# Performance work log

Measured on AMD Instinct MI355X. Metric: run time of the kernel, lower is better.

## Reference

```python
import jax, jax.numpy as jnp
import numpy as np

B, N, C, R, E = 8, 4096, 128, 16, 65536


def setup_inputs() -> dict:
    key = jax.random.key(0)
    ks = jax.random.split(key, 8)
    node_features = jax.random.normal(ks[0], (B, N, C), dtype=jnp.float32)
    edge_index = jax.random.randint(ks[1], (B, 2, E), 0, N, dtype=jnp.int64)
    edge_type = jax.random.randint(ks[2], (B, E), 0, R, dtype=jnp.int64)
    s = 1.0 / np.sqrt(C)
    rel_weight = jax.random.uniform(ks[3], (R, C, C), jnp.float32, -s, s)
    root_weight = jax.random.uniform(ks[4], (C, C), jnp.float32, -s, s)
    rgcn_bias = jnp.zeros((C,), jnp.float32)
    lin_weight = jax.random.uniform(ks[5], (C, 1), jnp.float32, -s, s)
    lin_bias = jnp.zeros((1,), jnp.float32)
    return {
        'node_features': node_features,
        'edge_index': edge_index,
        'edge_type': edge_type,
        'rel_weight': rel_weight,
        'root_weight': root_weight,
        'rgcn_bias': rgcn_bias,
        'lin_weight': lin_weight,
        'lin_bias': lin_bias,
    }


def _rgcn_score(node_features, edge_index, edge_type, rel_weight, root_weight,
                rgcn_bias, lin_weight, lin_bias):
    # Flatten batch of graphs into one big disjoint graph (as batch_rgcn does).
    x = node_features.reshape(B * N, C)
    offs = (jnp.arange(B, dtype=edge_index.dtype) * N)[:, None, None]  # (B,1,1)
    ei = (edge_index + offs).transpose(1, 0, 2).reshape(2, B * E)  # (2, B*E)
    et = edge_type.reshape(B * E)
    src, dst = ei[0], ei[1]

    x_src = x[src]  # (B*E, C) gathered source features
    # root transform + bias (RGCNConv root_weight + bias)
    out = x @ root_weight + rgcn_bias  # (B*N, C)
    # per-relation mean aggregation; mean(W_r x_j) == W_r mean(x_j)
    for r in range(R):
        mask = (et == r).astype(x.dtype)  # (B*E,)
        s = jax.ops.segment_sum(x_src * mask[:, None], dst, num_segments=B * N)
        cnt = jax.ops.segment_sum(mask, dst, num_segments=B * N)
        mean = jnp.where(cnt[:, None] > 0, s / jnp.maximum(cnt, 1.0)[:, None], 0.0)
        out = out + mean @ rel_weight[r]

    out = jax.nn.relu(out)  # dropout is identity at eval
    scores = (out @ lin_weight + lin_bias).reshape(B, N)
    return scores


def reference(node_features, edge_index, edge_type, rel_weight, root_weight,
              rgcn_bias, lin_weight, lin_bias):
    return _rgcn_score(node_features, edge_index, edge_type, rel_weight,
                       root_weight, rgcn_bias, lin_weight, lin_bias)
```

## Files before the change

### kernel.cpp

```cpp
#include <hip/hip_runtime.h>

#define BB 8
#define NN 4096
#define CC 128
#define RR 16
#define EE 65536
#define NNODES 32768
#define NEDGES 524288
#define BCAP  48
#define SCAP  16
#define NT    32
#define ALP   136

typedef unsigned short ushort_t;
typedef short bf16x8 __attribute__((ext_vector_type(8)));
typedef float f32x4 __attribute__((ext_vector_type(4)));

__device__ __forceinline__ unsigned short f2b(float f) {
    unsigned u = __builtin_bit_cast(unsigned, f);
    unsigned r = (u + 0x7fffu + ((u >> 16) & 1u)) >> 16;
    return (unsigned short)r;
}
__device__ __forceinline__ float b2f(unsigned short s) {
    return __builtin_bit_cast(float, (unsigned)s << 16);
}
__device__ __forceinline__ float ldf(const void* p, int j, int isbf) {
    return isbf ? b2f(((const ushort_t*)p)[j]) : ((const float*)p)[j];
}
__device__ __forceinline__ int ldi(const int* p, int j, int is64) {
    return p[j << is64];
}
__device__ __forceinline__ unsigned cvtpk(float lo, float hi) {
    unsigned r;
    asm("v_cvt_pk_bf16_f32 %0, %1, %2" : "=v"(r) : "v"(lo), "v"(hi));
    return r;
}

__device__ __forceinline__ int probe_isbf(const ushort_t* xf) {
    int t = threadIdx.x & 63;
    int bad = 0;
    for (int j = t; j < 512; j += 64) {
        unsigned e = (xf[j] >> 7) & 0xffu;
        if (e >= 160u) bad = 1;
    }
    return __ballot(bad) == 0ull;
}

#define GATHER_SUM(u, sb) do { \
    s[sb+0] += __builtin_bit_cast(float, (u).x << 16); \
    s[sb+1] += __builtin_bit_cast(float, (u).x & 0xffff0000u); \
    s[sb+2] += __builtin_bit_cast(float, (u).y << 16); \
    s[sb+3] += __builtin_bit_cast(float, (u).y & 0xffff0000u); \
    s[sb+4] += __builtin_bit_cast(float, (u).z << 16); \
    s[sb+5] += __builtin_bit_cast(float, (u).z & 0xffff0000u); \
    s[sb+6] += __builtin_bit_cast(float, (u).w << 16); \
    s[sb+7] += __builtin_bit_cast(float, (u).w & 0xffff0000u); \
} while (0)

__global__ __launch_bounds__(256) void prep_k(const void* __restrict__ x,
                                              const void* __restrict__ relw,
                                              const void* __restrict__ rootw,
                                              const int* __restrict__ ei,
                                              const int* __restrict__ et,
                                              ushort_t* __restrict__ Xb,
                                              ushort_t* __restrict__ WT3,
                                              int* __restrict__ dcnt,
                                              int* __restrict__ bucket,
                                              int* __restrict__ flags) {
    int bx = blockIdx.x, t = threadIdx.x;
    if (bx < 512) {
        int lane = t & 63;
        int pa = (lane < 16) ? ei[2 * lane + 1] : 0;
        int pb = (lane < 16) ? et[2 * lane + 1] : 0;
        int w64i = (__ballot(pa != 0) == 0ull);
        int w64t = (__ballot(pb != 0) == 0ull);
        int b = bx & 7;
        #pragma unroll
        for (int i = 0; i < 4; ++i) {
            int e = (bx >> 3) * 1024 + i * 256 + t;
            int src = ldi(ei, (b * 2) * EE + e, w64i);
            int dst = ldi(ei, (b * 2 + 1) * EE + e, w64i);
            int r = ldi(et, (b << 16) + e, w64t);
            int gd = (b << 12) + dst;
            int pos = atomicAdd(&dcnt[gd], 1);
            if (pos < BCAP)
                bucket[gd * BCAP + pos] = (((b << 12) + src) << 4) | r;
        }
    } else if (bx < 1024) {
        int isbf = probe_isbf((const ushort_t*)x);
        int bx2 = bx - 512;
        int base = (bx2 & 7) * 65536 + (bx2 >> 3) * 256 + t;
        #pragma unroll
        for (int i = 0; i < 4; ++i) {
            int tid = base + i * 16384;
            if (isbf) {
                ((uint4*)Xb)[tid] = ((const uint4*)x)[tid];
            } else {
                const float4* xf = (const float4*)x;
                float4 a = xf[2 * tid], b = xf[2 * tid + 1];
                ushort4 o0, o1;
                o0.x = f2b(a.x); o0.y = f2b(a.y); o0.z = f2b(a.z); o0.w = f2b(a.w);
                o1.x = f2b(b.x); o1.y = f2b(b.y); o1.z = f2b(b.z); o1.w = f2b(b.w);
                ((ushort4*)Xb)[2 * tid] = o0; ((ushort4*)Xb)[2 * tid + 1] = o1;
            }
        }
    } else {
        __shared__ ushort_t Ls[128 * 40];
        int isbf = probe_isbf((const ushort_t*)x);
        int mb = bx - 1024;
        int mat = mb >> 2, chunk = mb & 3;
        const void* src = (mat == 16) ? rootw : relw;
        int soff = (mat == 16) ? 0 : mat * 16384;
        int k0 = chunk * 32;
        #pragma unroll
        for (int i = 0; i < 16; ++i) {
            int idx = t + i * 256;
            int k = idx >> 7, c = idx & 127;
            Ls[c * 40 + k] = f2b(ldf(src, soff + (k0 + k) * 128 + c, isbf));
        }
        __syncthreads();
        #pragma unroll
        for (int i = 0; i < 2; ++i) {
            int idx = t + i * 256;
            int cg = idx >> 6, lane = idx & 63;
            int lrow = lane & 15, lq = lane >> 4;
            uint4 v = *(const uint4*)(&Ls[(cg * 16 + lrow) * 40 + lq * 8]);
            *(uint4*)(WT3 + ((size_t)((mat * 4 + chunk) * 8 + cg)) * 512 + lane * 8) = v;
        }
        if (mb == 0 && t == 0) flags[0] = isbf;
    }
}

__global__ __launch_bounds__(256, 4) void agg_k(const ushort_t* __restrict__ Xb,
                                                const ushort_t* __restrict__ WT3,
                                                const int* __restrict__ dcnt,
                                                const int* __restrict__ bucket,
                                                const void* __restrict__ bias,
                                                const void* __restrict__ linw,
                                                const void* __restrict__ linb,
                                                void* __restrict__ out,
                                                const int* __restrict__ flags) {
    __shared__ int scnt[NT * 16];
    __shared__ ushort_t srt[NT * 16 * SCAP];
    __shared__ ushort_t A[2][NT * ALP];
    __shared__ float red[NT][5];
    int bx = blockIdx.x, t = threadIdx.x;
    int isbf = flags[0];
    int n0 = (bx & 7) * NN + (bx >> 3) * NT;

    scnt[t] = 0; scnt[256 + t] = 0;
    __syncthreads();

    int nsub = t >> 3, tsub = t & 7;
    int gn = n0 + nsub;
    int offA = tsub * 8, offB = 64 + tsub * 8;
    int nc = dcnt[gn]; if (nc > BCAP) nc = BCAP;
    const int* bk = bucket + gn * BCAP;
    for (int j = tsub; j < nc; j += 8) {
        int v = bk[j];
        int pos = atomicAdd(&scnt[(nsub << 4) + (v & 15)], 1);
        if (pos < SCAP)
            srt[(((nsub << 4) + (v & 15)) << 4) + pos] = (ushort_t)((unsigned)v >> 4);
    }
    __syncthreads();

    int wave = t >> 6, lane = t & 63, lrow = lane & 15, lq = lane >> 4;
    f32x4 acc[2][2] = {};

    {
        int cf = scnt[nsub << 4];
        int ce = cf > SCAP ? SCAP : cf;
        const ushort_t* lst = &srt[nsub << 8];
        float s[16];
        #pragma unroll
        for (int j = 0; j < 16; ++j) s[j] = 0.f;
        for (int e = 0; e < ce; ++e) {
            const ushort_t* xr = Xb + (size_t)lst[e] * 128;
            uint4 ua = *(const uint4*)(xr + offA), ub = *(const uint4*)(xr + offB);
            GATHER_SUM(ua, 0); GATHER_SUM(ub, 8);
        }
        float w = (cf > 0) ? 1.0f / (float)cf : 0.f;
        uint4 va, vb;
        va.x = cvtpk(s[0] * w, s[1] * w);   va.y = cvtpk(s[2] * w, s[3] * w);
        va.z = cvtpk(s[4] * w, s[5] * w);   va.w = cvtpk(s[6] * w, s[7] * w);
        vb.x = cvtpk(s[8] * w, s[9] * w);   vb.y = cvtpk(s[10] * w, s[11] * w);
        vb.z = cvtpk(s[12] * w, s[13] * w); vb.w = cvtpk(s[14] * w, s[15] * w);
        *(uint4*)(&A[0][nsub * ALP + offA]) = va;
        *(uint4*)(&A[0][nsub * ALP + offB]) = vb;
    }
    __syncthreads();

    for (int p = 0; p < 17; ++p) {
        int np = p + 1;
        uint4 r0a, r0b, r1a, r1b, r2a, r2b, r3a, r3b;
        int cf = 0, ce = 0;
        if (np < 16) {
            cf = scnt[(nsub << 4) + np];
            ce = cf > SCAP ? SCAP : cf;
            uint4 q0 = *(const uint4*)(&srt[((nsub << 4) + np) << 4]);
            int e0 = q0.x & 0xffffu, e1 = q0.x >> 16;
            int e2i = q0.y & 0xffffu, e3 = q0.y >> 16;
            if (ce > 0) { const ushort_t* xr = Xb + (size_t)e0 * 128;  r0a = *(const uint4*)(xr + offA); r0b = *(const uint4*)(xr + offB); }
            if (ce > 1) { const ushort_t* xr = Xb + (size_t)e1 * 128;  r1a = *(const uint4*)(xr + offA); r1b = *(const uint4*)(xr + offB); }
            if (ce > 2) { const ushort_t* xr = Xb + (size_t)e2i * 128; r2a = *(const uint4*)(xr + offA); r2b = *(const uint4*)(xr + offB); }
            if (ce > 3) { const ushort_t* xr = Xb + (size_t)e3 * 128;  r3a = *(const uint4*)(xr + offA); r3b = *(const uint4*)(xr + offB); }
        } else if (np == 16) {
            const ushort_t* xr = Xb + (size_t)gn * 128;
            r0a = *(const uint4*)(xr + offA); r0b = *(const uint4*)(xr + offB);
        }
        const ushort_t* Ap = A[p & 1];
        const ushort_t* bw = WT3 + (size_t)p * 16384 + (wave * 2) * 512 + lane * 8;
        __builtin_amdgcn_s_setprio(1);
        #pragma unroll
        for (int ks = 0; ks < 4; ++ks) {
            int k0 = ks * 32 + lq * 8;
            bf16x8 a0 = *(const bf16x8*)(&Ap[lrow * ALP + k0]);
            bf16x8 a1 = *(const bf16x8*)(&Ap[(16 + lrow) * ALP + k0]);
            bf16x8 b0 = *(const bf16x8*)(bw + ks * 4096);
            bf16x8 b1 = *(const bf16x8*)(bw + ks * 4096 + 512);
            acc[0][0] = __builtin_amdgcn_mfma_f32_16x16x32_bf16(a0, b0, acc[0][0], 0, 0, 0);
            acc[0][1] = __builtin_amdgcn_mfma_f32_16x16x32_bf16(a0, b1, acc[0][1], 0, 0, 0);
            acc[1][0] = __builtin_amdgcn_mfma_f32_16x16x32_bf16(a1, b0, acc[1][0], 0, 0, 0);
            acc[1][1] = __builtin_amdgcn_mfma_f32_16x16x32_bf16(a1, b1, acc[1][1], 0, 0, 0);
        }
        __builtin_amdgcn_s_setprio(0);
        if (np < 16) {
            float s[16];
            #pragma unroll
            for (int j = 0; j < 16; ++j) s[j] = 0.f;
            if (ce > 0) { GATHER_SUM(r0a, 0); GATHER_SUM(r0b, 8); }
            if (ce > 1) { GATHER_SUM(r1a, 0); GATHER_SUM(r1b, 8); }
            if (ce > 2) { GATHER_SUM(r2a, 0); GATHER_SUM(r2b, 8); }
            if (ce > 3) { GATHER_SUM(r3a, 0); GATHER_SUM(r3b, 8); }
            if (ce > 4) {
                const ushort_t* lst = &srt[((nsub << 4) + np) << 4];
                for (int e4 = 4; e4 < ce; ++e4) {
                    const ushort_t* xr = Xb + (size_t)lst[e4] * 128;
                    uint4 ta = *(const uint4*)(xr + offA), tb = *(const uint4*)(xr + offB);
                    GATHER_SUM(ta, 0); GATHER_SUM(tb, 8);
                }
            }
            float w = (cf > 0) ? 1.0f / (float)cf : 0.f;
            uint4 va, vb;
            va.x = cvtpk(s[0] * w, s[1] * w);   va.y = cvtpk(s[2] * w, s[3] * w);
            va.z = cvtpk(s[4] * w, s[5] * w);   va.w = cvtpk(s[6] * w, s[7] * w);
            vb.x = cvtpk(s[8] * w, s[9] * w);   vb.y = cvtpk(s[10] * w, s[11] * w);
            vb.z = cvtpk(s[12] * w, s[13] * w); vb.w = cvtpk(s[14] * w, s[15] * w);
            *(uint4*)(&A[np & 1][nsub * ALP + offA]) = va;
            *(uint4*)(&A[np & 1][nsub * ALP + offB]) = vb;
        } else if (np == 16) {
            *(uint4*)(&A[np & 1][nsub * ALP + offA]) = r0a;
            *(uint4*)(&A[np & 1][nsub * ALP + offB]) = r0b;
        }
        if (p < 16) __syncthreads();
    }

    int wn = wave << 5;
    int c0 = wn + lrow, c1 = wn + 16 + lrow;
    float bi0 = ldf(bias, c0, isbf), bi1 = ldf(bias, c1, isbf);
    float lw0 = ldf(linw, c0, isbf), lw1 = ldf(linw, c1, isbf);
    #pragma unroll
    for (int mi = 0; mi < 2; ++mi)
        #pragma unroll
        for (int rg = 0; rg < 4; ++rg) {
            float p = fmaxf(acc[mi][0][rg] + bi0, 0.f) * lw0
                    + fmaxf(acc[mi][1][rg] + bi1, 0.f) * lw1;
            p += __shfl_xor(p, 1, 64);
            p += __shfl_xor(p, 2, 64);
            p += __shfl_xor(p, 4, 64);
            p += __shfl_xor(p, 8, 64);
            if (lrow == 0) red[mi * 16 + lq * 4 + rg][wave] = p;
        }
    __syncthreads();
    if (t < NT) {
        float res = red[t][0] + red[t][1] + red[t][2] + red[t][3] + ldf(linb, 0, isbf);
        if (isbf) ((ushort_t*)out)[n0 + t] = f2b(res);
        else      ((float*)out)[n0 + t] = res;
    }
}

extern "C" void kernel_launch(void* const* d_in, const int* in_sizes, int n_in,
                              void* d_out, int out_size, void* d_ws, size_t ws_size,
                              hipStream_t stream) {
    const void* x     = d_in[0];
    const int*  ei    = (const int*)d_in[1];
    const int*  et    = (const int*)d_in[2];
    const void* relw  = d_in[3];
    const void* rootw = d_in[4];
    const void* bias  = d_in[5];
    const void* linw  = d_in[6];
    const void* linb  = d_in[7];

    const size_t WS_NEED = 15368448;
    if (ws_size < WS_NEED) return;

    char* ws = (char*)d_ws;
    ushort_t* Xb     = (ushort_t*)(ws);
    ushort_t* WT3    = (ushort_t*)(ws + 8388608);
    int*      dcnt   = (int*)(ws + 8945664);
    int*      bucket = (int*)(ws + 9076736);
    int*      flags  = (int*)(ws + 15368192);

    hipMemsetAsync(dcnt, 0, 131072, stream);
    prep_k<<<1092, 256, 0, stream>>>(x, relw, rootw, ei, et, Xb, WT3, dcnt, bucket, flags);
    agg_k<<<1024, 256, 0, stream>>>(Xb, WT3, dcnt, bucket, bias, linw, linb, d_out, flags);
}
```

Before: 144.4 us.

## Fuse prep and aggregation into one persistent kernel with grid barriers

```diff
diff --git a/kernel.cpp b/kernel.cpp
--- a/kernel.cpp
+++ b/kernel.cpp
@@ -8,9 +8,10 @@
 #define NNODES 32768
 #define NEDGES 524288
 #define BCAP  48
-#define SCAP  16
+#define SCE   15
 #define NT    32
 #define ALP   136
+#define NBLK  1024
 
 typedef unsigned short ushort_t;
 typedef short bf16x8 __attribute__((ext_vector_type(8)));
@@ -36,17 +37,7 @@
     return r;
 }
 
-__device__ __forceinline__ int probe_isbf(const ushort_t* xf) {
-    int t = threadIdx.x & 63;
-    int bad = 0;
-    for (int j = t; j < 512; j += 64) {
-        unsigned e = (xf[j] >> 7) & 0xffu;
-        if (e >= 160u) bad = 1;
-    }
-    return __ballot(bad) == 0ull;
-}
-
-#define GATHER_SUM(u, sb) do { \
+#define GSUM8(u, sb) do { \
     s[sb+0] += __builtin_bit_cast(float, (u).x << 16); \
     s[sb+1] += __builtin_bit_cast(float, (u).x & 0xffff0000u); \
     s[sb+2] += __builtin_bit_cast(float, (u).y << 16); \
@@ -57,127 +48,131 @@
     s[sb+7] += __builtin_bit_cast(float, (u).w & 0xffff0000u); \
 } while (0)
 
-__global__ __launch_bounds__(256) void prep_k(const void* __restrict__ x,
-                                              const void* __restrict__ relw,
-                                              const void* __restrict__ rootw,
-                                              const int* __restrict__ ei,
-                                              const int* __restrict__ et,
-                                              ushort_t* __restrict__ Xb,
-                                              ushort_t* __restrict__ WT3,
-                                              int* __restrict__ dcnt,
-                                              int* __restrict__ bucket,
-                                              int* __restrict__ flags) {
-    int bx = blockIdx.x, t = threadIdx.x;
-    if (bx < 512) {
-        int lane = t & 63;
-        int pa = (lane < 16) ? ei[2 * lane + 1] : 0;
-        int pb = (lane < 16) ? et[2 * lane + 1] : 0;
-        int w64i = (__ballot(pa != 0) == 0ull);
-        int w64t = (__ballot(pb != 0) == 0ull);
-        int b = bx & 7;
-        #pragma unroll
-        for (int i = 0; i < 4; ++i) {
-            int e = (bx >> 3) * 1024 + i * 256 + t;
-            int src = ldi(ei, (b * 2) * EE + e, w64i);
-            int dst = ldi(ei, (b * 2 + 1) * EE + e, w64i);
-            int r = ldi(et, (b << 16) + e, w64t);
-            int gd = (b << 12) + dst;
-            int pos = atomicAdd(&dcnt[gd], 1);
-            if (pos < BCAP)
-                bucket[gd * BCAP + pos] = (((b << 12) + src) << 4) | r;
-        }
-    } else if (bx < 1024) {
-        int isbf = probe_isbf((const ushort_t*)x);
-        int bx2 = bx - 512;
-        int base = (bx2 & 7) * 65536 + (bx2 >> 3) * 256 + t;
-        #pragma unroll
-        for (int i = 0; i < 4; ++i) {
-            int tid = base + i * 16384;
-            if (isbf) {
-                ((uint4*)Xb)[tid] = ((const uint4*)x)[tid];
-            } else {
-                const float4* xf = (const float4*)x;
-                float4 a = xf[2 * tid], b = xf[2 * tid + 1];
-                ushort4 o0, o1;
-                o0.x = f2b(a.x); o0.y = f2b(a.y); o0.z = f2b(a.z); o0.w = f2b(a.w);
-                o1.x = f2b(b.x); o1.y = f2b(b.y); o1.z = f2b(b.z); o1.w = f2b(b.w);
-                ((ushort4*)Xb)[2 * tid] = o0; ((ushort4*)Xb)[2 * tid + 1] = o1;
-            }
-        }
-    } else {
-        __shared__ ushort_t Ls[128 * 40];
-        int isbf = probe_isbf((const ushort_t*)x);
-        int mb = bx - 1024;
-        int mat = mb >> 2, chunk = mb & 3;
-        const void* src = (mat == 16) ? rootw : relw;
-        int soff = (mat == 16) ? 0 : mat * 16384;
-        int k0 = chunk * 32;
-        #pragma unroll
-        for (int i = 0; i < 16; ++i) {
-            int idx = t + i * 256;
-            int k = idx >> 7, c = idx & 127;
-            Ls[c * 40 + k] = f2b(ldf(src, soff + (k0 + k) * 128 + c, isbf));
-        }
-        __syncthreads();
-        #pragma unroll
-        for (int i = 0; i < 2; ++i) {
-            int idx = t + i * 256;
-            int cg = idx >> 6, lane = idx & 63;
-            int lrow = lane & 15, lq = lane >> 4;
-            uint4 v = *(const uint4*)(&Ls[(cg * 16 + lrow) * 40 + lq * 8]);
-            *(uint4*)(WT3 + ((size_t)((mat * 4 + chunk) * 8 + cg)) * 512 + lane * 8) = v;
-        }
-        if (mb == 0 && t == 0) flags[0] = isbf;
-    }
-}
-
-__global__ __launch_bounds__(256, 4) void agg_k(const ushort_t* __restrict__ Xb,
-                                                const ushort_t* __restrict__ WT3,
-                                                const int* __restrict__ dcnt,
-                                                const int* __restrict__ bucket,
-                                                const void* __restrict__ bias,
-                                                const void* __restrict__ linw,
-                                                const void* __restrict__ linb,
-                                                void* __restrict__ out,
-                                                const int* __restrict__ flags) {
-    __shared__ int scnt[NT * 16];
-    __shared__ ushort_t srt[NT * 16 * SCAP];
-    __shared__ ushort_t A[2][NT * ALP];
-    __shared__ float red[NT][5];
-    int bx = blockIdx.x, t = threadIdx.x;
-    int isbf = flags[0];
+struct AggSM {
+    int scnt[NT * 16];
+    ushort_t srt[NT * 16 * 16];
+    ushort_t A[2][NT * ALP];
+    float red[NT][5];
+};
+union SM {
+    AggSM agg;
+    ushort_t Ls[128 * 40];
+};
+
+__device__ __forceinline__ void gbar(int* bar, int idx) {
+    __syncthreads();
+    if (threadIdx.x == 0) {
+        __threadfence();
+        atomicAdd(&bar[idx * 16], 1);
+        while (atomicAdd(&bar[idx * 16], 0) < NBLK)
+            __builtin_amdgcn_s_sleep(8);
+        __threadfence();
+    }
+    __syncthreads();
+}
+
+__device__ __forceinline__ void do_cast(int bx, int t, const void* x,
+                                        ushort_t* Xb, int isbf) {
+    int base = (bx & 7) * 65536 + (bx >> 3) * 512 + t;
+    #pragma unroll
+    for (int i = 0; i < 2; ++i) {
+        int tid = base + i * 256;
+        if (isbf) {
+            ((uint4*)Xb)[tid] = ((const uint4*)x)[tid];
+        } else {
+            const float4* xf = (const float4*)x;
+            float4 a = xf[2 * tid], b = xf[2 * tid + 1];
+            ushort4 o0, o1;
+            o0.x = f2b(a.x); o0.y = f2b(a.y); o0.z = f2b(a.z); o0.w = f2b(a.w);
+            o1.x = f2b(b.x); o1.y = f2b(b.y); o1.z = f2b(b.z); o1.w = f2b(b.w);
+            ((ushort4*)Xb)[2 * tid] = o0; ((ushort4*)Xb)[2 * tid + 1] = o1;
+        }
+    }
+}
+
+__device__ __forceinline__ void do_wt3(int mb, int t, ushort_t* Ls,
+                                       const void* relw, const void* rootw,
+                                       ushort_t* WT3, int isbf) {
+    int mat = mb >> 2, chunk = mb & 3;
+    const void* src = (mat == 16) ? rootw : relw;
+    int soff = (mat == 16) ? 0 : mat * 16384;
+    int k0 = chunk * 32;
+    #pragma unroll
+    for (int i = 0; i < 16; ++i) {
+        int idx = t + i * 256;
+        int k = idx >> 7, c = idx & 127;
+        Ls[c * 40 + k] = f2b(ldf(src, soff + (k0 + k) * 128 + c, isbf));
+    }
+    __syncthreads();
+    #pragma unroll
+    for (int i = 0; i < 2; ++i) {
+        int idx = t + i * 256;
+        int cg = idx >> 6, lane = idx & 63;
+        int lrow = lane & 15, lq = lane >> 4;
+        uint4 v = *(const uint4*)(&Ls[(cg * 16 + lrow) * 40 + lq * 8]);
+        *(uint4*)(WT3 + ((size_t)((mat * 4 + chunk) * 8 + cg)) * 512 + lane * 8) = v;
+    }
+}
+
+__device__ __forceinline__ void do_edges(int bx, int t, const int* ei, const int* et,
+                                         int* dcnt, int* bucket, int w64i, int w64t) {
+    int b = bx & 7;
+    int e0 = (bx >> 3) * 512 + t, e1 = e0 + 256;
+    int src0 = ldi(ei, (b * 2) * EE + e0, w64i);
+    int dst0 = ldi(ei, (b * 2 + 1) * EE + e0, w64i);
+    int r0 = ldi(et, (b << 16) + e0, w64t);
+    int src1 = ldi(ei, (b * 2) * EE + e1, w64i);
+    int dst1 = ldi(ei, (b * 2 + 1) * EE + e1, w64i);
+    int r1 = ldi(et, (b << 16) + e1, w64t);
+    int gd0 = (b << 12) + dst0, gd1 = (b << 12) + dst1;
+    int p0 = atomicAdd(&dcnt[gd0 << 4], 1);
+    int p1 = atomicAdd(&dcnt[gd1 << 4], 1);
+    if (p0 < BCAP) bucket[gd0 * BCAP + p0] = (((b << 12) + src0) << 4) | r0;
+    if (p1 < BCAP) bucket[gd1 * BCAP + p1] = (((b << 12) + src1) << 4) | r1;
+}
+
+__device__ __forceinline__ void do_agg(int bx, int t, AggSM& sm,
+                                       const ushort_t* Xb, const ushort_t* WT3,
+                                       const int* dcnt, const int* bucket,
+                                       const void* bias, const void* linw,
+                                       const void* linb, void* out, int isbf) {
     int n0 = (bx & 7) * NN + (bx >> 3) * NT;
 
-    scnt[t] = 0; scnt[256 + t] = 0;
+    sm.scnt[t] = 0; sm.scnt[256 + t] = 0;
     __syncthreads();
 
     int nsub = t >> 3, tsub = t & 7;
     int gn = n0 + nsub;
     int offA = tsub * 8, offB = 64 + tsub * 8;
-    int nc = dcnt[gn]; if (nc > BCAP) nc = BCAP;
+    int nc = dcnt[gn << 4]; if (nc > BCAP) nc = BCAP;
     const int* bk = bucket + gn * BCAP;
     for (int j = tsub; j < nc; j += 8) {
         int v = bk[j];
-        int pos = atomicAdd(&scnt[(nsub << 4) + (v & 15)], 1);
-        if (pos < SCAP)
-            srt[(((nsub << 4) + (v & 15)) << 4) + pos] = (ushort_t)((unsigned)v >> 4);
-    }
+        int row = (nsub << 4) + (v & 15);
+        int pos = atomicAdd(&sm.scnt[row], 1);
+        if (pos < SCE)
+            sm.srt[(row << 4) + 1 + pos] = (ushort_t)((unsigned)v >> 4);
+    }
+    __syncthreads();
+    sm.srt[t << 4] = (ushort_t)sm.scnt[t];
+    sm.srt[(t + 256) << 4] = (ushort_t)sm.scnt[t + 256];
     __syncthreads();
 
     int wave = t >> 6, lane = t & 63, lrow = lane & 15, lq = lane >> 4;
     f32x4 acc[2][2] = {};
 
     {
-        int cf = scnt[nsub << 4];
-        int ce = cf > SCAP ? SCAP : cf;
-        const ushort_t* lst = &srt[nsub << 8];
+        int row = nsub << 4;
+        uint4 q0 = *(const uint4*)(&sm.srt[row << 4]);
+        int cf = q0.x & 0xffffu; int ce = cf > SCE ? SCE : cf;
         float s[16];
         #pragma unroll
         for (int j = 0; j < 16; ++j) s[j] = 0.f;
         for (int e = 0; e < ce; ++e) {
-            const ushort_t* xr = Xb + (size_t)lst[e] * 128;
+            int gs = sm.srt[(row << 4) + 1 + e];
+            const ushort_t* xr = Xb + (size_t)gs * 128;
             uint4 ua = *(const uint4*)(xr + offA), ub = *(const uint4*)(xr + offB);
-            GATHER_SUM(ua, 0); GATHER_SUM(ub, 8);
+            GSUM8(ua, 0); GSUM8(ub, 8);
         }
         float w = (cf > 0) ? 1.0f / (float)cf : 0.f;
         uint4 va, vb;
@@ -185,30 +180,29 @@
         va.z = cvtpk(s[4] * w, s[5] * w);   va.w = cvtpk(s[6] * w, s[7] * w);
         vb.x = cvtpk(s[8] * w, s[9] * w);   vb.y = cvtpk(s[10] * w, s[11] * w);
         vb.z = cvtpk(s[12] * w, s[13] * w); vb.w = cvtpk(s[14] * w, s[15] * w);
-        *(uint4*)(&A[0][nsub * ALP + offA]) = va;
-        *(uint4*)(&A[0][nsub * ALP + offB]) = vb;
+        *(uint4*)(&sm.A[0][nsub * ALP + offA]) = va;
+        *(uint4*)(&sm.A[0][nsub * ALP + offB]) = vb;
     }
     __syncthreads();
 
     for (int p = 0; p < 17; ++p) {
         int np = p + 1;
         uint4 r0a, r0b, r1a, r1b, r2a, r2b, r3a, r3b;
-        int cf = 0, ce = 0;
+        int cf = 0, ce = 0, row = 0;
         if (np < 16) {
-            cf = scnt[(nsub << 4) + np];
-            ce = cf > SCAP ? SCAP : cf;
-            uint4 q0 = *(const uint4*)(&srt[((nsub << 4) + np) << 4]);
-            int e0 = q0.x & 0xffffu, e1 = q0.x >> 16;
-            int e2i = q0.y & 0xffffu, e3 = q0.y >> 16;
-            if (ce > 0) { const ushort_t* xr = Xb + (size_t)e0 * 128;  r0a = *(const uint4*)(xr + offA); r0b = *(const uint4*)(xr + offB); }
-            if (ce > 1) { const ushort_t* xr = Xb + (size_t)e1 * 128;  r1a = *(const uint4*)(xr + offA); r1b = *(const uint4*)(xr + offB); }
-            if (ce > 2) { const ushort_t* xr = Xb + (size_t)e2i * 128; r2a = *(const uint4*)(xr + offA); r2b = *(const uint4*)(xr + offB); }
-            if (ce > 3) { const ushort_t* xr = Xb + (size_t)e3 * 128;  r3a = *(const uint4*)(xr + offA); r3b = *(const uint4*)(xr + offB); }
+            row = (nsub << 4) + np;
+            uint4 q0 = *(const uint4*)(&sm.srt[row << 4]);
+            cf = q0.x & 0xffffu; ce = cf > SCE ? SCE : cf;
+            int e0 = q0.x >> 16, e1 = q0.y & 0xffffu, e2 = q0.y >> 16, e3 = q0.z & 0xffffu;
+            if (ce > 0) { const ushort_t* xr = Xb + (size_t)e0 * 128; r0a = *(const uint4*)(xr + offA); r0b = *(const uint4*)(xr + offB); }
+            if (ce > 1) { const ushort_t* xr = Xb + (size_t)e1 * 128; r1a = *(const uint4*)(xr + offA); r1b = *(const uint4*)(xr + offB); }
+            if (ce > 2) { const ushort_t* xr = Xb + (size_t)e2 * 128; r2a = *(const uint4*)(xr + offA); r2b = *(const uint4*)(xr + offB); }
+            if (ce > 3) { const ushort_t* xr = Xb + (size_t)e3 * 128; r3a = *(const uint4*)(xr + offA); r3b = *(const uint4*)(xr + offB); }
         } else if (np == 16) {
             const ushort_t* xr = Xb + (size_t)gn * 128;
             r0a = *(const uint4*)(xr + offA); r0b = *(const uint4*)(xr + offB);
         }
-        const ushort_t* Ap = A[p & 1];
+        const ushort_t* Ap = sm.A[p & 1];
         const ushort_t* bw = WT3 + (size_t)p * 16384 + (wave * 2) * 512 + lane * 8;
         __builtin_amdgcn_s_setprio(1);
         #pragma unroll
@@ -228,16 +222,16 @@
             float s[16];
             #pragma unroll
             for (int j = 0; j < 16; ++j) s[j] = 0.f;
-            if (ce > 0) { GATHER_SUM(r0a, 0); GATHER_SUM(r0b, 8); }
-            if (ce > 1) { GATHER_SUM(r1a, 0); GATHER_SUM(r1b, 8); }
-            if (ce > 2) { GATHER_SUM(r2a, 0); GATHER_SUM(r2b, 8); }
-            if (ce > 3) { GATHER_SUM(r3a, 0); GATHER_SUM(r3b, 8); }
+            if (ce > 0) { GSUM8(r0a, 0); GSUM8(r0b, 8); }
+            if (ce > 1) { GSUM8(r1a, 0); GSUM8(r1b, 8); }
+            if (ce > 2) { GSUM8(r2a, 0); GSUM8(r2b, 8); }
+            if (ce > 3) { GSUM8(r3a, 0); GSUM8(r3b, 8); }
             if (ce > 4) {
-                const ushort_t* lst = &srt[((nsub << 4) + np) << 4];
                 for (int e4 = 4; e4 < ce; ++e4) {
-                    const ushort_t* xr = Xb + (size_t)lst[e4] * 128;
+                    int gs = sm.srt[(row << 4) + 1 + e4];
+                    const ushort_t* xr = Xb + (size_t)gs * 128;
                     uint4 ta = *(const uint4*)(xr + offA), tb = *(const uint4*)(xr + offB);
-                    GATHER_SUM(ta, 0); GATHER_SUM(tb, 8);
+                    GSUM8(ta, 0); GSUM8(tb, 8);
                 }
             }
             float w = (cf > 0) ? 1.0f / (float)cf : 0.f;
@@ -246,11 +240,11 @@
             va.z = cvtpk(s[4] * w, s[5] * w);   va.w = cvtpk(s[6] * w, s[7] * w);
             vb.x = cvtpk(s[8] * w, s[9] * w);   vb.y = cvtpk(s[10] * w, s[11] * w);
             vb.z = cvtpk(s[12] * w, s[13] * w); vb.w = cvtpk(s[14] * w, s[15] * w);
-            *(uint4*)(&A[np & 1][nsub * ALP + offA]) = va;
-            *(uint4*)(&A[np & 1][nsub * ALP + offB]) = vb;
+            *(uint4*)(&sm.A[np & 1][nsub * ALP + offA]) = va;
+            *(uint4*)(&sm.A[np & 1][nsub * ALP + offB]) = vb;
         } else if (np == 16) {
-            *(uint4*)(&A[np & 1][nsub * ALP + offA]) = r0a;
-            *(uint4*)(&A[np & 1][nsub * ALP + offB]) = r0b;
+            *(uint4*)(&sm.A[np & 1][nsub * ALP + offA]) = r0a;
+            *(uint4*)(&sm.A[np & 1][nsub * ALP + offB]) = r0b;
         }
         if (p < 16) __syncthreads();
     }
@@ -269,14 +263,44 @@
             p += __shfl_xor(p, 2, 64);
             p += __shfl_xor(p, 4, 64);
             p += __shfl_xor(p, 8, 64);
-            if (lrow == 0) red[mi * 16 + lq * 4 + rg][wave] = p;
+            if (lrow == 0) sm.red[mi * 16 + lq * 4 + rg][wave] = p;
         }
     __syncthreads();
     if (t < NT) {
-        float res = red[t][0] + red[t][1] + red[t][2] + red[t][3] + ldf(linb, 0, isbf);
+        float res = sm.red[t][0] + sm.red[t][1] + sm.red[t][2] + sm.red[t][3]
+                  + ldf(linb, 0, isbf);
         if (isbf) ((ushort_t*)out)[n0 + t] = f2b(res);
         else      ((float*)out)[n0 + t] = res;
     }
+}
+
+__global__ __launch_bounds__(256, 4) void fused_k(const void* __restrict__ x,
+                                                  const void* __restrict__ relw,
+                                                  const void* __restrict__ rootw,
+                                                  const int* __restrict__ ei,
+                                                  const int* __restrict__ et,
+                                                  ushort_t* __restrict__ Xb,
+                                                  ushort_t* __restrict__ WT3,
+                                                  int* __restrict__ dcnt,
+                                                  int* __restrict__ bucket,
+                                                  int* __restrict__ bar,
+                                                  const void* __restrict__ bias,
+                                                  const void* __restrict__ linw,
+                                                  const void* __restrict__ linb,
+                                                  void* __restrict__ out,
+                                                  int isbf, int w64i, int w64t) {
+    __shared__ SM sm;
+    int bx = blockIdx.x, t = threadIdx.x;
+
+    if (t < 128) ((uint4*)dcnt)[(bx << 7) + t] = make_uint4(0, 0, 0, 0);
+    do_cast(bx, t, x, Xb, isbf);
+    if (bx < 68) do_wt3(bx, t, sm.Ls, relw, rootw, WT3, isbf);
+    gbar(bar, 0);
+
+    do_edges(bx, t, ei, et, dcnt, bucket, w64i, w64t);
+    gbar(bar, 1);
+
+    do_agg(bx, t, sm.agg, Xb, WT3, dcnt, bucket, bias, linw, linb, out, isbf);
 }
 
 extern "C" void kernel_launch(void* const* d_in, const int* in_sizes, int n_in,
@@ -291,17 +315,21 @@
     const void* linw  = d_in[6];
     const void* linb  = d_in[7];
 
-    const size_t WS_NEED = 15368448;
+    int isbf = (in_sizes[0] == BB * NN * CC * 2);
+    int w64i = (in_sizes[1] == BB * 2 * EE * 8);
+    int w64t = (in_sizes[2] == BB * EE * 8);
+
+    const size_t WS_NEED = 17334528;
     if (ws_size < WS_NEED) return;
 
     char* ws = (char*)d_ws;
     ushort_t* Xb     = (ushort_t*)(ws);
     ushort_t* WT3    = (ushort_t*)(ws + 8388608);
     int*      dcnt   = (int*)(ws + 8945664);
-    int*      bucket = (int*)(ws + 9076736);
-    int*      flags  = (int*)(ws + 15368192);
-
-    hipMemsetAsync(dcnt, 0, 131072, stream);
-    prep_k<<<1092, 256, 0, stream>>>(x, relw, rootw, ei, et, Xb, WT3, dcnt, bucket, flags);
-    agg_k<<<1024, 256, 0, stream>>>(Xb, WT3, dcnt, bucket, bias, linw, linb, d_out, flags);
-}
+    int*      bucket = (int*)(ws + 11042816);
+    int*      bar    = (int*)(ws + 17334272);
+
+    hipMemsetAsync(bar, 0, 256, stream);
+    fused_k<<<NBLK, 256, 0, stream>>>(x, relw, rootw, ei, et, Xb, WT3, dcnt, bucket,
+                                      bar, bias, linw, linb, d_out, isbf, w64i, w64t);
+}
```

New measurement: 381.3 us. 2.64x slower.

## Warp-specialize aggregation into gather and MFMA waves, pad counters, host-side dtype detection

Applied to the files above, without the earlier changes.

```diff
diff --git a/kernel.cpp b/kernel.cpp
--- a/kernel.cpp
+++ b/kernel.cpp
@@ -8,7 +8,7 @@
 #define NNODES 32768
 #define NEDGES 524288
 #define BCAP  48
-#define SCAP  16
+#define SCE   15
 #define NT    32
 #define ALP   136
 
@@ -36,17 +36,7 @@
     return r;
 }
 
-__device__ __forceinline__ int probe_isbf(const ushort_t* xf) {
-    int t = threadIdx.x & 63;
-    int bad = 0;
-    for (int j = t; j < 512; j += 64) {
-        unsigned e = (xf[j] >> 7) & 0xffu;
-        if (e >= 160u) bad = 1;
-    }
-    return __ballot(bad) == 0ull;
-}
-
-#define GATHER_SUM(u, sb) do { \
+#define GSUM8(u, sb) do { \
     s[sb+0] += __builtin_bit_cast(float, (u).x << 16); \
     s[sb+1] += __builtin_bit_cast(float, (u).x & 0xffff0000u); \
     s[sb+2] += __builtin_bit_cast(float, (u).y << 16); \
@@ -66,14 +56,9 @@
                                               ushort_t* __restrict__ WT3,
                                               int* __restrict__ dcnt,
                                               int* __restrict__ bucket,
-                                              int* __restrict__ flags) {
+                                              int isbf, int w64i, int w64t) {
     int bx = blockIdx.x, t = threadIdx.x;
     if (bx < 512) {
-        int lane = t & 63;
-        int pa = (lane < 16) ? ei[2 * lane + 1] : 0;
-        int pb = (lane < 16) ? et[2 * lane + 1] : 0;
-        int w64i = (__ballot(pa != 0) == 0ull);
-        int w64t = (__ballot(pb != 0) == 0ull);
         int b = bx & 7;
         #pragma unroll
         for (int i = 0; i < 4; ++i) {
@@ -82,12 +67,11 @@
             int dst = ldi(ei, (b * 2 + 1) * EE + e, w64i);
             int r = ldi(et, (b << 16) + e, w64t);
             int gd = (b << 12) + dst;
-            int pos = atomicAdd(&dcnt[gd], 1);
+            int pos = atomicAdd(&dcnt[gd << 4], 1);
             if (pos < BCAP)
                 bucket[gd * BCAP + pos] = (((b << 12) + src) << 4) | r;
         }
     } else if (bx < 1024) {
-        int isbf = probe_isbf((const ushort_t*)x);
         int bx2 = bx - 512;
         int base = (bx2 & 7) * 65536 + (bx2 >> 3) * 256 + t;
         #pragma unroll
@@ -106,7 +90,6 @@
         }
     } else {
         __shared__ ushort_t Ls[128 * 40];
-        int isbf = probe_isbf((const ushort_t*)x);
         int mb = bx - 1024;
         int mat = mb >> 2, chunk = mb & 3;
         const void* src = (mat == 16) ? rootw : relw;
@@ -127,11 +110,10 @@
             uint4 v = *(const uint4*)(&Ls[(cg * 16 + lrow) * 40 + lq * 8]);
             *(uint4*)(WT3 + ((size_t)((mat * 4 + chunk) * 8 + cg)) * 512 + lane * 8) = v;
         }
-        if (mb == 0 && t == 0) flags[0] = isbf;
-    }
-}
-
-__global__ __launch_bounds__(256, 4) void agg_k(const ushort_t* __restrict__ Xb,
+    }
+}
+
+__global__ __launch_bounds__(512, 4) void agg_k(const ushort_t* __restrict__ Xb,
                                                 const ushort_t* __restrict__ WT3,
                                                 const int* __restrict__ dcnt,
                                                 const int* __restrict__ bucket,
@@ -139,45 +121,53 @@
                                                 const void* __restrict__ linw,
                                                 const void* __restrict__ linb,
                                                 void* __restrict__ out,
-                                                const int* __restrict__ flags) {
+                                                int isbf) {
     __shared__ int scnt[NT * 16];
-    __shared__ ushort_t srt[NT * 16 * SCAP];
+    __shared__ ushort_t srt[NT * 16 * 16];
     __shared__ ushort_t A[2][NT * ALP];
     __shared__ float red[NT][5];
     int bx = blockIdx.x, t = threadIdx.x;
-    int isbf = flags[0];
     int n0 = (bx & 7) * NN + (bx >> 3) * NT;
 
-    scnt[t] = 0; scnt[256 + t] = 0;
-    __syncthreads();
-
-    int nsub = t >> 3, tsub = t & 7;
+    scnt[t & 511] = 0;
+    __syncthreads();
+
+    {
+        int ns16 = t >> 4, ts16 = t & 15;
+        int gn16 = n0 + ns16;
+        int nc = dcnt[gn16 << 4]; if (nc > BCAP) nc = BCAP;
+        const int* bk = bucket + gn16 * BCAP;
+        for (int j = ts16; j < nc; j += 16) {
+            int v = bk[j];
+            int row = (ns16 << 4) + (v & 15);
+            int pos = atomicAdd(&scnt[row], 1);
+            if (pos < SCE)
+                srt[(row << 4) + 1 + pos] = (ushort_t)((unsigned)v >> 4);
+        }
+    }
+    __syncthreads();
+    srt[t << 4] = (ushort_t)scnt[t];
+    __syncthreads();
+
+    int wave = t >> 6, lane = t & 63, lrow = lane & 15, lq = lane >> 4;
+    int tg = t & 255;
+    int nsub = tg >> 3, tsub = tg & 7;
     int gn = n0 + nsub;
     int offA = tsub * 8, offB = 64 + tsub * 8;
-    int nc = dcnt[gn]; if (nc > BCAP) nc = BCAP;
-    const int* bk = bucket + gn * BCAP;
-    for (int j = tsub; j < nc; j += 8) {
-        int v = bk[j];
-        int pos = atomicAdd(&scnt[(nsub << 4) + (v & 15)], 1);
-        if (pos < SCAP)
-            srt[(((nsub << 4) + (v & 15)) << 4) + pos] = (ushort_t)((unsigned)v >> 4);
-    }
-    __syncthreads();
-
-    int wave = t >> 6, lane = t & 63, lrow = lane & 15, lq = lane >> 4;
     f32x4 acc[2][2] = {};
 
-    {
-        int cf = scnt[nsub << 4];
-        int ce = cf > SCAP ? SCAP : cf;
-        const ushort_t* lst = &srt[nsub << 8];
+    if (wave >= 4) {
+        int row = nsub << 4;
+        uint4 q0 = *(const uint4*)(&srt[row << 4]);
+        int cf = q0.x & 0xffffu; int ce = cf > SCE ? SCE : cf;
         float s[16];
         #pragma unroll
         for (int j = 0; j < 16; ++j) s[j] = 0.f;
         for (int e = 0; e < ce; ++e) {
-            const ushort_t* xr = Xb + (size_t)lst[e] * 128;
+            int gs = srt[(row << 4) + 1 + e];
+            const ushort_t* xr = Xb + (size_t)gs * 128;
             uint4 ua = *(const uint4*)(xr + offA), ub = *(const uint4*)(xr + offB);
-            GATHER_SUM(ua, 0); GATHER_SUM(ub, 8);
+            GSUM8(ua, 0); GSUM8(ub, 8);
         }
         float w = (cf > 0) ? 1.0f / (float)cf : 0.f;
         uint4 va, vb;
@@ -192,52 +182,46 @@
 
     for (int p = 0; p < 17; ++p) {
         int np = p + 1;
-        uint4 r0a, r0b, r1a, r1b, r2a, r2b, r3a, r3b;
-        int cf = 0, ce = 0;
-        if (np < 16) {
-            cf = scnt[(nsub << 4) + np];
-            ce = cf > SCAP ? SCAP : cf;
-            uint4 q0 = *(const uint4*)(&srt[((nsub << 4) + np) << 4]);
-            int e0 = q0.x & 0xffffu, e1 = q0.x >> 16;
-            int e2i = q0.y & 0xffffu, e3 = q0.y >> 16;
-            if (ce > 0) { const ushort_t* xr = Xb + (size_t)e0 * 128;  r0a = *(const uint4*)(xr + offA); r0b = *(const uint4*)(xr + offB); }
-            if (ce > 1) { const ushort_t* xr = Xb + (size_t)e1 * 128;  r1a = *(const uint4*)(xr + offA); r1b = *(const uint4*)(xr + offB); }
-            if (ce > 2) { const ushort_t* xr = Xb + (size_t)e2i * 128; r2a = *(const uint4*)(xr + offA); r2b = *(const uint4*)(xr + offB); }
-            if (ce > 3) { const ushort_t* xr = Xb + (size_t)e3 * 128;  r3a = *(const uint4*)(xr + offA); r3b = *(const uint4*)(xr + offB); }
-        } else if (np == 16) {
-            const ushort_t* xr = Xb + (size_t)gn * 128;
-            r0a = *(const uint4*)(xr + offA); r0b = *(const uint4*)(xr + offB);
-        }
-        const ushort_t* Ap = A[p & 1];
-        const ushort_t* bw = WT3 + (size_t)p * 16384 + (wave * 2) * 512 + lane * 8;
-        __builtin_amdgcn_s_setprio(1);
-        #pragma unroll
-        for (int ks = 0; ks < 4; ++ks) {
-            int k0 = ks * 32 + lq * 8;
-            bf16x8 a0 = *(const bf16x8*)(&Ap[lrow * ALP + k0]);
-            bf16x8 a1 = *(const bf16x8*)(&Ap[(16 + lrow) * ALP + k0]);
-            bf16x8 b0 = *(const bf16x8*)(bw + ks * 4096);
-            bf16x8 b1 = *(const bf16x8*)(bw + ks * 4096 + 512);
-            acc[0][0] = __builtin_amdgcn_mfma_f32_16x16x32_bf16(a0, b0, acc[0][0], 0, 0, 0);
-            acc[0][1] = __builtin_amdgcn_mfma_f32_16x16x32_bf16(a0, b1, acc[0][1], 0, 0, 0);
-            acc[1][0] = __builtin_amdgcn_mfma_f32_16x16x32_bf16(a1, b0, acc[1][0], 0, 0, 0);
-            acc[1][1] = __builtin_amdgcn_mfma_f32_16x16x32_bf16(a1, b1, acc[1][1], 0, 0, 0);
-        }
-        __builtin_amdgcn_s_setprio(0);
-        if (np < 16) {
+        if (wave < 4) {
+            const ushort_t* Ap = A[p & 1];
+            const ushort_t* bw = WT3 + (size_t)p * 16384 + (wave * 2) * 512 + lane * 8;
+            __builtin_amdgcn_s_setprio(1);
+            #pragma unroll
+            for (int ks = 0; ks < 4; ++ks) {
+                int k0 = ks * 32 + lq * 8;
+                bf16x8 a0 = *(const bf16x8*)(&Ap[lrow * ALP + k0]);
+                bf16x8 a1 = *(const bf16x8*)(&Ap[(16 + lrow) * ALP + k0]);
+                bf16x8 b0 = *(const bf16x8*)(bw + ks * 4096);
+                bf16x8 b1 = *(const bf16x8*)(bw + ks * 4096 + 512);
+                acc[0][0] = __builtin_amdgcn_mfma_f32_16x16x32_bf16(a0, b0, acc[0][0], 0, 0, 0);
+                acc[0][1] = __builtin_amdgcn_mfma_f32_16x16x32_bf16(a0, b1, acc[0][1], 0, 0, 0);
+                acc[1][0] = __builtin_amdgcn_mfma_f32_16x16x32_bf16(a1, b0, acc[1][0], 0, 0, 0);
+                acc[1][1] = __builtin_amdgcn_mfma_f32_16x16x32_bf16(a1, b1, acc[1][1], 0, 0, 0);
+            }
+            __builtin_amdgcn_s_setprio(0);
+        } else if (np < 16) {
+            int row = (nsub << 4) + np;
+            uint4 q0 = *(const uint4*)(&srt[row << 4]);
+            int cf = q0.x & 0xffffu; int ce = cf > SCE ? SCE : cf;
+            int e0 = q0.x >> 16, e1 = q0.y & 0xffffu, e2 = q0.y >> 16, e3 = q0.z & 0xffffu;
+            uint4 r0a, r0b, r1a, r1b, r2a, r2b, r3a, r3b;
+            if (ce > 0) { const ushort_t* xr = Xb + (size_t)e0 * 128; r0a = *(const uint4*)(xr + offA); r0b = *(const uint4*)(xr + offB); }
+            if (ce > 1) { const ushort_t* xr = Xb + (size_t)e1 * 128; r1a = *(const uint4*)(xr + offA); r1b = *(const uint4*)(xr + offB); }
+            if (ce > 2) { const ushort_t* xr = Xb + (size_t)e2 * 128; r2a = *(const uint4*)(xr + offA); r2b = *(const uint4*)(xr + offB); }
+            if (ce > 3) { const ushort_t* xr = Xb + (size_t)e3 * 128; r3a = *(const uint4*)(xr + offA); r3b = *(const uint4*)(xr + offB); }
             float s[16];
             #pragma unroll
             for (int j = 0; j < 16; ++j) s[j] = 0.f;
-            if (ce > 0) { GATHER_SUM(r0a, 0); GATHER_SUM(r0b, 8); }
-            if (ce > 1) { GATHER_SUM(r1a, 0); GATHER_SUM(r1b, 8); }
-            if (ce > 2) { GATHER_SUM(r2a, 0); GATHER_SUM(r2b, 8); }
-            if (ce > 3) { GATHER_SUM(r3a, 0); GATHER_SUM(r3b, 8); }
+            if (ce > 0) { GSUM8(r0a, 0); GSUM8(r0b, 8); }
+            if (ce > 1) { GSUM8(r1a, 0); GSUM8(r1b, 8); }
+            if (ce > 2) { GSUM8(r2a, 0); GSUM8(r2b, 8); }
+            if (ce > 3) { GSUM8(r3a, 0); GSUM8(r3b, 8); }
             if (ce > 4) {
-                const ushort_t* lst = &srt[((nsub << 4) + np) << 4];
                 for (int e4 = 4; e4 < ce; ++e4) {
-                    const ushort_t* xr = Xb + (size_t)lst[e4] * 128;
+                    int gs = srt[(row << 4) + 1 + e4];
+                    const ushort_t* xr = Xb + (size_t)gs * 128;
                     uint4 ta = *(const uint4*)(xr + offA), tb = *(const uint4*)(xr + offB);
-                    GATHER_SUM(ta, 0); GATHER_SUM(tb, 8);
+                    GSUM8(ta, 0); GSUM8(tb, 8);
                 }
             }
             float w = (cf > 0) ? 1.0f / (float)cf : 0.f;
@@ -249,28 +233,32 @@
             *(uint4*)(&A[np & 1][nsub * ALP + offA]) = va;
             *(uint4*)(&A[np & 1][nsub * ALP + offB]) = vb;
         } else if (np == 16) {
+            const ushort_t* xr = Xb + (size_t)gn * 128;
+            uint4 r0a = *(const uint4*)(xr + offA), r0b = *(const uint4*)(xr + offB);
             *(uint4*)(&A[np & 1][nsub * ALP + offA]) = r0a;
             *(uint4*)(&A[np & 1][nsub * ALP + offB]) = r0b;
         }
         if (p < 16) __syncthreads();
     }
 
-    int wn = wave << 5;
-    int c0 = wn + lrow, c1 = wn + 16 + lrow;
-    float bi0 = ldf(bias, c0, isbf), bi1 = ldf(bias, c1, isbf);
-    float lw0 = ldf(linw, c0, isbf), lw1 = ldf(linw, c1, isbf);
-    #pragma unroll
-    for (int mi = 0; mi < 2; ++mi)
-        #pragma unroll
-        for (int rg = 0; rg < 4; ++rg) {
-            float p = fmaxf(acc[mi][0][rg] + bi0, 0.f) * lw0
-                    + fmaxf(acc[mi][1][rg] + bi1, 0.f) * lw1;
-            p += __shfl_xor(p, 1, 64);
-            p += __shfl_xor(p, 2, 64);
-            p += __shfl_xor(p, 4, 64);
-            p += __shfl_xor(p, 8, 64);
-            if (lrow == 0) red[mi * 16 + lq * 4 + rg][wave] = p;
-        }
+    if (wave < 4) {
+        int wn = wave << 5;
+        int c0 = wn + lrow, c1 = wn + 16 + lrow;
+        float bi0 = ldf(bias, c0, isbf), bi1 = ldf(bias, c1, isbf);
+        float lw0 = ldf(linw, c0, isbf), lw1 = ldf(linw, c1, isbf);
+        #pragma unroll
+        for (int mi = 0; mi < 2; ++mi)
+            #pragma unroll
+            for (int rg = 0; rg < 4; ++rg) {
+                float p = fmaxf(acc[mi][0][rg] + bi0, 0.f) * lw0
+                        + fmaxf(acc[mi][1][rg] + bi1, 0.f) * lw1;
+                p += __shfl_xor(p, 1, 64);
+                p += __shfl_xor(p, 2, 64);
+                p += __shfl_xor(p, 4, 64);
+                p += __shfl_xor(p, 8, 64);
+                if (lrow == 0) red[mi * 16 + lq * 4 + rg][wave] = p;
+            }
+    }
     __syncthreads();
     if (t < NT) {
         float res = red[t][0] + red[t][1] + red[t][2] + red[t][3] + ldf(linb, 0, isbf);
@@ -291,17 +279,21 @@
     const void* linw  = d_in[6];
     const void* linb  = d_in[7];
 
-    const size_t WS_NEED = 15368448;
+    int isbf = (in_sizes[0] == BB * NN * CC * 2);
+    int w64i = (in_sizes[1] == BB * 2 * EE * 8);
+    int w64t = (in_sizes[2] == BB * EE * 8);
+
+    const size_t WS_NEED = 17334272;
     if (ws_size < WS_NEED) return;
 
     char* ws = (char*)d_ws;
     ushort_t* Xb     = (ushort_t*)(ws);
     ushort_t* WT3    = (ushort_t*)(ws + 8388608);
     int*      dcnt   = (int*)(ws + 8945664);
-    int*      bucket = (int*)(ws + 9076736);
-    int*      flags  = (int*)(ws + 15368192);
-
-    hipMemsetAsync(dcnt, 0, 131072, stream);
-    prep_k<<<1092, 256, 0, stream>>>(x, relw, rootw, ei, et, Xb, WT3, dcnt, bucket, flags);
-    agg_k<<<1024, 256, 0, stream>>>(Xb, WT3, dcnt, bucket, bias, linw, linb, d_out, flags);
-}
+    int*      bucket = (int*)(ws + 11042816);
+
+    hipMemsetAsync(dcnt, 0, 2097152, stream);
+    prep_k<<<1092, 256, 0, stream>>>(x, relw, rootw, ei, et, Xb, WT3, dcnt, bucket,
+                                     isbf, w64i, w64t);
+    agg_k<<<1024, 512, 0, stream>>>(Xb, WT3, dcnt, bucket, bias, linw, linb, d_out, isbf);
+}
```

New measurement: 153.6 us. 1.06x slower.
